# Kernel optimization log

Hardware: AMD Instinct MI355X
Metric: run time of the kernel (lower is better)

Reference implementation:

```python
import math
import jax, jax.numpy as jnp
import numpy as np

B, NW, WH, WW, C, NH = 1024, 64, 8, 8, 512, 8
N = WH * WW
HD = C // NH


def _rel_tables():
    # log-spaced continuous relative coords, shape [(2wh-1)*(2ww-1), 2]
    rh = np.arange(-(WH - 1), WH, dtype=np.float32)
    rw = np.arange(-(WW - 1), WW, dtype=np.float32)
    g = np.stack(np.meshgrid(rh, rw, indexing='ij'), axis=-1)
    norm = np.array([max(WH - 1, 1), max(WW - 1, 1)], dtype=np.float32)
    g = g / norm * 8.0
    g = np.sign(g) * np.log2(np.abs(g) + 1.0) / math.log2(9.0)
    rel_coords = g.reshape(-1, 2).astype(np.float32)
    # relative position index table, shape [N, N]
    ch = np.arange(WH)
    cw = np.arange(WW)
    coords = np.stack(np.meshgrid(ch, cw, indexing='ij')).reshape(2, -1)  # [2, N]
    idx = coords[:, :, None] - coords[:, None, :]  # [2, N, N]
    idx = idx.transpose(1, 2, 0).copy()
    idx[:, :, 0] += WH - 1
    idx[:, :, 1] += WW - 1
    idx[:, :, 0] *= 2 * WW - 1
    rel_idx = idx.sum(-1).astype(np.int32)  # [N, N]
    return jnp.asarray(rel_coords), jnp.asarray(rel_idx)

_REL_COORDS, _REL_IDX = _rel_tables()


def setup_inputs() -> dict:
    key = jax.random.key(0)
    ks = jax.random.split(key, 8)
    x = jax.random.normal(ks[0], (B, N, C), dtype=jnp.float32)
    mask = jnp.zeros((NW, N, N), dtype=jnp.float32)
    qkv_w = jax.random.normal(ks[1], (3 * C, C), dtype=jnp.float32) * 0.02
    q_bias = jnp.zeros((C,), dtype=jnp.float32)
    v_bias = jnp.zeros((C,), dtype=jnp.float32)
    logit_scale = jnp.full((NH, 1, 1), math.log(10.0), dtype=jnp.float32)
    cpb_w1 = jax.random.normal(ks[2], (512, 2), dtype=jnp.float32) * 0.02
    cpb_b1 = jnp.zeros((512,), dtype=jnp.float32)
    cpb_w2 = jax.random.normal(ks[3], (NH, 512), dtype=jnp.float32) * 0.02
    proj_w = jax.random.normal(ks[4], (C, C), dtype=jnp.float32) * 0.02
    proj_b = jnp.zeros((C,), dtype=jnp.float32)
    return {"x": x, "mask": mask, "qkv_w": qkv_w, "q_bias": q_bias,
            "v_bias": v_bias, "logit_scale": logit_scale, "cpb_w1": cpb_w1,
            "cpb_b1": cpb_b1, "cpb_w2": cpb_w2, "proj_w": proj_w,
            "proj_b": proj_b}


def reference(x, mask, qkv_w, q_bias, v_bias, logit_scale,
              cpb_w1, cpb_b1, cpb_w2, proj_w, proj_b):
    # qkv with q/v bias only (k bias is zero)
    bias = jnp.concatenate([q_bias, jnp.zeros_like(v_bias), v_bias])
    qkv = x @ qkv_w.T + bias  # [B, N, 3C]
    qkv = qkv.reshape(B, N, 3, NH, HD).transpose(2, 0, 3, 1, 4)  # [3, B, NH, N, HD]
    q, k, v = qkv[0], qkv[1], qkv[2]
    # cosine-similarity attention with clamped per-head log scale
    q = q / jnp.maximum(jnp.linalg.norm(q, axis=-1, keepdims=True), 1e-12)
    k = k / jnp.maximum(jnp.linalg.norm(k, axis=-1, keepdims=True), 1e-12)
    scale = jnp.exp(jnp.minimum(logit_scale, math.log(100.0)))  # [NH,1,1]
    attn = jnp.einsum('bhnd,bhmd->bhnm', q, k) * scale  # [B, NH, N, N]
    # continuous relative position bias via 2-layer MLP
    cpb = jax.nn.relu(_REL_COORDS @ cpb_w1.T + cpb_b1) @ cpb_w2.T  # [(2wh-1)(2ww-1), NH]
    cpb = 16.0 * jax.nn.sigmoid(cpb)
    bias_mat = cpb[_REL_IDX.reshape(-1)].reshape(N, N, NH).transpose(2, 0, 1)  # [NH, N, N]
    attn = attn + bias_mat[None]
    # window mask add: group windows per image
    attn = attn.reshape(B // NW, NW, NH, N, N) + mask[None, :, None]
    attn = attn.reshape(B, NH, N, N)
    attn = jax.nn.softmax(attn, axis=-1)
    out = jnp.einsum('bhnm,bhmd->bnhd', attn, v).reshape(B, N, C)
    return out @ proj_w.T + proj_b
```

## Files before the change

### kernel.cpp

```cpp
#include <hip/hip_runtime.h>


typedef __bf16 bf16;
typedef bf16  bf16x8 __attribute__((ext_vector_type(8)));
typedef float f32x4  __attribute__((ext_vector_type(4)));

#define MFMA16(a, b, c) __builtin_amdgcn_mfma_f32_16x16x32_bf16((a), (b), (c), 0, 0, 0)

__device__ __forceinline__ unsigned short f2bf_bits(float f) {
  return __builtin_bit_cast(unsigned short, (bf16)f);
}

__device__ __forceinline__ void gload_lds16(const void* g, void* l) {
  __builtin_amdgcn_global_load_lds(
      (const __attribute__((address_space(1))) void*)g,
      (__attribute__((address_space(3))) void*)l, 16, 0, 0);
}

#define OFF_CPB     0u
#define OFF_QKVWT   8192u
#define OFF_PROJWT  1581056u
#define OFF_QHAT    2105344u
#define OFF_KHAT    69214208u
#define OFF_VT      136323072u
#define OFF_ATTN    203431936u
#define OFF_XT      OFF_ATTN

__global__ void wconv_kernel(const float* __restrict__ qkvw,
                             const float* __restrict__ projw,
                             char* __restrict__ ws) {
  int i = blockIdx.x * 256 + threadIdx.x;
#pragma unroll
  for (int it = 0; it < 4; ++it) {
    int idx = i + it * 65536;
    const float* src;
    unsigned base;
    int row, c4;
    if (idx < 196608) {
      row = idx >> 7; c4 = idx & 127;
      src = qkvw + row * 512 + c4 * 4;
      base = OFF_QKVWT + (unsigned)(((row >> 7) * 8 + (c4 >> 4)) << 14);
    } else {
      int j = idx - 196608;
      row = j >> 7; c4 = j & 127;
      src = projw + row * 512 + c4 * 4;
      base = OFF_PROJWT + (unsigned)(((row >> 7) * 8 + (c4 >> 4)) << 14);
    }
    int n = row & 127;
    int kb = (c4 & 15) * 8;
    float4 v = *(const float4*)src;
    ushort4 o;
    o.x = f2bf_bits(v.x); o.y = f2bf_bits(v.y);
    o.z = f2bf_bits(v.z); o.w = f2bf_bits(v.w);
    *(ushort4*)(ws + base + n * 128 + (kb ^ ((n & 7) << 4))) = o;
  }
}

__global__ void xconv_kernel(const float* __restrict__ x, char* __restrict__ ws) {
  int i = blockIdx.x * 1024 + threadIdx.x;
#pragma unroll
  for (int it = 0; it < 4; ++it) {
    int idx = i + it * 256;
    int row = idx >> 7, c4 = idx & 127;
    float4 v = *((const float4*)x + idx);
    ushort4 o;
    o.x = f2bf_bits(v.x); o.y = f2bf_bits(v.y);
    o.z = f2bf_bits(v.z); o.w = f2bf_bits(v.w);
    int n = row & 127;
    int kb = (c4 & 15) * 8;
    size_t base = OFF_XT + ((size_t)((row >> 7) * 8 + (c4 >> 4)) << 14);
    *(ushort4*)(ws + base + n * 128 + (kb ^ ((n & 7) << 4))) = o;
  }
}

__global__ void cpb_kernel(const float* __restrict__ w1, const float* __restrict__ b1,
                           const float* __restrict__ w2, float* __restrict__ cpb_small) {
  const int t = blockIdx.x;
  const int tid = threadIdx.x;
  const int a = t / 15, bb = t % 15;
  const float rh = (float)(a - 7) * (8.0f / 7.0f);
  const float rw = (float)(bb - 7) * (8.0f / 7.0f);
  const float inv_log2_9 = 0.3154648767971186f;
  float sh = (rh > 0.f) ? 1.f : ((rh < 0.f) ? -1.f : 0.f);
  float sw = (rw > 0.f) ? 1.f : ((rw < 0.f) ? -1.f : 0.f);
  float c0 = sh * log2f(fabsf(rh) + 1.0f) * inv_log2_9;
  float c1 = sw * log2f(fabsf(rw) + 1.0f) * inv_log2_9;
  float acc[8] = {0, 0, 0, 0, 0, 0, 0, 0};
  for (int j = tid; j < 512; j += 256) {
    float hv = fmaf(c0, w1[2 * j], fmaf(c1, w1[2 * j + 1], b1[j]));
    hv = fmaxf(hv, 0.0f);
#pragma unroll
    for (int hh = 0; hh < 8; ++hh) acc[hh] = fmaf(hv, w2[hh * 512 + j], acc[hh]);
  }
#pragma unroll
  for (int hh = 0; hh < 8; ++hh)
#pragma unroll
    for (int s = 1; s < 64; s <<= 1) acc[hh] += __shfl_xor(acc[hh], s, 64);
  __shared__ float wsum[4][8];
  if ((tid & 63) == 0) {
#pragma unroll
    for (int hh = 0; hh < 8; ++hh) wsum[tid >> 6][hh] = acc[hh];
  }
  __syncthreads();
  if (tid < 8) {
    float s = wsum[0][tid] + wsum[1][tid] + wsum[2][tid] + wsum[3][tid];
    cpb_small[t * 8 + tid] = 16.0f / (1.0f + expf(-s));
  }
}

__launch_bounds__(256)
__global__ void qkv_gemm(const float* __restrict__ q_bias,
                         const float* __restrict__ v_bias,
                         char* __restrict__ ws) {
  __shared__ __align__(16) char As[16384];
  __shared__ __align__(16) char Bs[16384];
  const int tid = threadIdx.x;
  const int w = tid >> 6, l = tid & 63, lg = l >> 4, lo = l & 15;
  const int wm = w >> 1, wn = w & 1;
  const int bid = blockIdx.x;
  const int wg = (bid & 7) * 768 + (bid >> 3);
  const int mb = wg / 12, nb = wg % 12;

  const char* at_base = ws + OFF_XT + ((size_t)mb * 8 << 14);
  const char* bt_base = ws + OFF_QKVWT + (unsigned)(nb * 8 << 14);

  f32x4 acc[4][4];
#pragma unroll
  for (int mt = 0; mt < 4; ++mt)
#pragma unroll
    for (int nt = 0; nt < 4; ++nt) { f32x4 z = {0.f, 0.f, 0.f, 0.f}; acc[mt][nt] = z; }

#pragma unroll 1
  for (int kc = 0; kc < 8; ++kc) {
    __syncthreads();
    const char* at = at_base + (kc << 14);
    const char* bt = bt_base + (kc << 14);
#pragma unroll
    for (int i = 0; i < 4; ++i) {
      int chunk = i * 4 + w;
      gload_lds16(at + chunk * 1024 + l * 16, As + chunk * 1024);
      gload_lds16(bt + chunk * 1024 + l * 16, Bs + chunk * 1024);
    }
    __syncthreads();
#pragma unroll
    for (int ks = 0; ks < 2; ++ks) {
      bf16x8 af[4], bf[4];
#pragma unroll
      for (int mt = 0; mt < 4; ++mt) {
        int m = wm * 64 + mt * 16 + lo;
        af[mt] = *(const bf16x8*)(As + m * 128 + ((ks * 64 + lg * 16) ^ ((m & 7) << 4)));
      }
#pragma unroll
      for (int nt = 0; nt < 4; ++nt) {
        int n = wn * 64 + nt * 16 + lo;
        bf[nt] = *(const bf16x8*)(Bs + n * 128 + ((ks * 64 + lg * 16) ^ ((n & 7) << 4)));
      }
#pragma unroll
      for (int mt = 0; mt < 4; ++mt)
#pragma unroll
        for (int nt = 0; nt < 4; ++nt)
          acc[mt][nt] = MFMA16(af[mt], bf[nt], acc[mt][nt]);
    }
  }

  const int mat = nb >> 2;
  const int h = ((nb & 3) << 1) + wn;
  const int win = mb * 2 + wm;
  const size_t hb = ((size_t)win * 8 + h) * 4096;

  if (mat != 1) {
    const float* bsrc = (mat == 0) ? q_bias : v_bias;
    float bias[4];
#pragma unroll
    for (int nt = 0; nt < 4; ++nt) bias[nt] = bsrc[h * 64 + nt * 16 + lo];
#pragma unroll
    for (int mt = 0; mt < 4; ++mt)
#pragma unroll
      for (int nt = 0; nt < 4; ++nt)
#pragma unroll
        for (int r = 0; r < 4; ++r) acc[mt][nt][r] += bias[nt];
  }

  if (mat < 2) {
    bf16* dst = (bf16*)(ws + (mat == 0 ? OFF_QHAT : OFF_KHAT)) + hb;
#pragma unroll
    for (int mt = 0; mt < 4; ++mt) {
#pragma unroll
      for (int r = 0; r < 4; ++r) {
        float ss = acc[mt][0][r] * acc[mt][0][r] + acc[mt][1][r] * acc[mt][1][r] +
                   acc[mt][2][r] * acc[mt][2][r] + acc[mt][3][r] * acc[mt][3][r];
#pragma unroll
        for (int s = 1; s < 16; s <<= 1) ss += __shfl_xor(ss, s, 64);
        float rinv = 1.0f / fmaxf(sqrtf(ss), 1e-12f);
        int tok = mt * 16 + lg * 4 + r;
#pragma unroll
        for (int nt = 0; nt < 4; ++nt)
          dst[tok * 64 + nt * 16 + lo] = (bf16)(acc[mt][nt][r] * rinv);
      }
    }
  } else {
    bf16* dst = (bf16*)(ws + OFF_VT) + hb;
#pragma unroll
    for (int mt = 0; mt < 4; ++mt) {
#pragma unroll
      for (int nt = 0; nt < 4; ++nt) {
        ushort4 o;
        o.x = f2bf_bits(acc[mt][nt][0]); o.y = f2bf_bits(acc[mt][nt][1]);
        o.z = f2bf_bits(acc[mt][nt][2]); o.w = f2bf_bits(acc[mt][nt][3]);
        int d = nt * 16 + lo, tok0 = mt * 16 + lg * 4;
        *(ushort4*)(dst + d * 64 + tok0) = o;
      }
    }
  }
}

__launch_bounds__(256)
__global__ void attn_kernel(const float* __restrict__ mask,
                            const float* __restrict__ logit_scale,
                            char* __restrict__ ws) {
  __shared__ float cpbs[1800];
  __shared__ __align__(16) char psb[4][8192];
  const int tid = threadIdx.x;
  const int w = tid >> 6, l = tid & 63, lg = l >> 4, lo = l & 15;
  const int b = blockIdx.x;
  const int widx = b & 63;

  const float* cpb_small = (const float*)(ws + OFF_CPB);
  for (int i = tid; i < 1800; i += 256) cpbs[i] = cpb_small[i];
  __syncthreads();

  const float* mrow = mask + widx * 4096;
  char* pw = psb[w];

#pragma unroll
  for (int hh = 0; hh < 2; ++hh) {
    const int h = w * 2 + hh;
    const size_t hb = ((size_t)b * 8 + h) * 4096;
    const bf16* qh = (const bf16*)(ws + OFF_QHAT) + hb;
    const bf16* kh = (const bf16*)(ws + OFF_KHAT) + hb;
    const bf16* vh = (const bf16*)(ws + OFF_VT) + hb;
    const float scale = __expf(fminf(logit_scale[h], 4.605170185988091f));

    f32x4 sacc[4][4];
#pragma unroll
    for (int mt = 0; mt < 4; ++mt)
#pragma unroll
      for (int nt = 0; nt < 4; ++nt) { f32x4 z = {0.f, 0.f, 0.f, 0.f}; sacc[mt][nt] = z; }
#pragma unroll
    for (int ks = 0; ks < 2; ++ks) {
      bf16x8 a4[4], b4[4];
#pragma unroll
      for (int mt = 0; mt < 4; ++mt)
        a4[mt] = *(const bf16x8*)(qh + (mt * 16 + lo) * 64 + ks * 32 + lg * 8);
#pragma unroll
      for (int nt = 0; nt < 4; ++nt)
        b4[nt] = *(const bf16x8*)(kh + (nt * 16 + lo) * 64 + ks * 32 + lg * 8);
#pragma unroll
      for (int mt = 0; mt < 4; ++mt)
#pragma unroll
        for (int nt = 0; nt < 4; ++nt)
          sacc[mt][nt] = MFMA16(a4[mt], b4[nt], sacc[mt][nt]);
    }

    float invl[4][4];
#pragma unroll
    for (int mt = 0; mt < 4; ++mt) {
#pragma unroll
      for (int r = 0; r < 4; ++r) {
        int row = mt * 16 + lg * 4 + r;
        float sv[4];
#pragma unroll
        for (int nt = 0; nt < 4; ++nt) {
          int col = nt * 16 + lo;
          int idx = ((row >> 3) - (col >> 3) + 7) * 15 + (row & 7) - (col & 7) + 7;
          sv[nt] = fmaf(sacc[mt][nt][r], scale, cpbs[idx * 8 + h] + mrow[row * 64 + col]);
        }
        float mr = fmaxf(fmaxf(sv[0], sv[1]), fmaxf(sv[2], sv[3]));
#pragma unroll
        for (int s = 1; s < 16; s <<= 1) mr = fmaxf(mr, __shfl_xor(mr, s, 64));
        float ls = 0.f;
#pragma unroll
        for (int nt = 0; nt < 4; ++nt) { sv[nt] = __expf(sv[nt] - mr); ls += sv[nt]; }
#pragma unroll
        for (int s = 1; s < 16; s <<= 1) ls += __shfl_xor(ls, s, 64);
        invl[mt][r] = 1.0f / ls;
#pragma unroll
        for (int nt = 0; nt < 4; ++nt)
          *(bf16*)(pw + row * 128 + (((nt * 16 + lo) * 2) ^ ((row & 7) << 4))) = (bf16)sv[nt];
      }
    }
    asm volatile("" ::: "memory");

    f32x4 oacc[4][4];
#pragma unroll
    for (int mt = 0; mt < 4; ++mt)
#pragma unroll
      for (int nt = 0; nt < 4; ++nt) { f32x4 z = {0.f, 0.f, 0.f, 0.f}; oacc[mt][nt] = z; }
#pragma unroll
    for (int ks = 0; ks < 2; ++ks) {
      bf16x8 pa[4], b4[4];
#pragma unroll
      for (int mt = 0; mt < 4; ++mt) {
        int m = mt * 16 + lo;
        pa[mt] = *(const bf16x8*)(pw + m * 128 + ((ks * 64 + lg * 16) ^ ((m & 7) << 4)));
      }
#pragma unroll
      for (int nt = 0; nt < 4; ++nt)
        b4[nt] = *(const bf16x8*)(vh + (nt * 16 + lo) * 64 + ks * 32 + lg * 8);
#pragma unroll
      for (int mt = 0; mt < 4; ++mt)
#pragma unroll
        for (int nt = 0; nt < 4; ++nt)
          oacc[mt][nt] = MFMA16(pa[mt], b4[nt], oacc[mt][nt]);
    }

    char* at = ws + OFF_ATTN + ((size_t)((b >> 1) * 8 + h) << 14);
#pragma unroll
    for (int mt = 0; mt < 4; ++mt) {
#pragma unroll
      for (int r = 0; r < 4; ++r) {
        int rt = (b & 1) * 64 + mt * 16 + lg * 4 + r;
#pragma unroll
        for (int nt = 0; nt < 4; ++nt) {
          int d = nt * 16 + lo;
          *(bf16*)(at + rt * 128 + ((d * 2) ^ ((rt & 7) << 4))) =
              (bf16)(oacc[mt][nt][r] * invl[mt][r]);
        }
      }
    }
    asm volatile("" ::: "memory");
  }
}

__launch_bounds__(256)
__global__ void proj_kernel(const float* __restrict__ proj_b,
                            float* __restrict__ out,
                            const char* __restrict__ ws) {
  __shared__ __align__(16) char As[16384];
  __shared__ __align__(16) char Bs[16384];
  const int tid = threadIdx.x;
  const int w = tid >> 6, l = tid & 63, lg = l >> 4, lo = l & 15;
  const int wm = w >> 1, wn = w & 1;
  const int bid = blockIdx.x;
  const int wg = (bid & 7) * 256 + (bid >> 3);
  const int mb = wg >> 2, nbp = wg & 3;

  const char* at_base = ws + OFF_ATTN + ((size_t)mb * 8 << 14);
  const char* bt_base = ws + OFF_PROJWT + (unsigned)(nbp * 8 << 14);

  f32x4 acc[4][4];
#pragma unroll
  for (int mt = 0; mt < 4; ++mt)
#pragma unroll
    for (int nt = 0; nt < 4; ++nt) { f32x4 z = {0.f, 0.f, 0.f, 0.f}; acc[mt][nt] = z; }

#pragma unroll 1
  for (int kc = 0; kc < 8; ++kc) {
    __syncthreads();
    const char* at = at_base + (kc << 14);
    const char* bt = bt_base + (kc << 14);
#pragma unroll
    for (int i = 0; i < 4; ++i) {
      int chunk = i * 4 + w;
      gload_lds16(at + chunk * 1024 + l * 16, As + chunk * 1024);
      gload_lds16(bt + chunk * 1024 + l * 16, Bs + chunk * 1024);
    }
    __syncthreads();
#pragma unroll
    for (int ks = 0; ks < 2; ++ks) {
      bf16x8 af[4], bf[4];
#pragma unroll
      for (int mt = 0; mt < 4; ++mt) {
        int m = wm * 64 + mt * 16 + lo;
        af[mt] = *(const bf16x8*)(As + m * 128 + ((ks * 64 + lg * 16) ^ ((m & 7) << 4)));
      }
#pragma unroll
      for (int nt = 0; nt < 4; ++nt) {
        int n = wn * 64 + nt * 16 + lo;
        bf[nt] = *(const bf16x8*)(Bs + n * 128 + ((ks * 64 + lg * 16) ^ ((n & 7) << 4)));
      }
#pragma unroll
      for (int mt = 0; mt < 4; ++mt)
#pragma unroll
        for (int nt = 0; nt < 4; ++nt)
          acc[mt][nt] = MFMA16(af[mt], bf[nt], acc[mt][nt]);
    }
  }
#pragma unroll
  for (int nt = 0; nt < 4; ++nt) {
    int col = nbp * 128 + wn * 64 + nt * 16 + lo;
    float pb = proj_b[col];
#pragma unroll
    for (int mt = 0; mt < 4; ++mt) {
#pragma unroll
      for (int r = 0; r < 4; ++r) {
        int row = mb * 128 + wm * 64 + mt * 16 + lg * 4 + r;
        out[(size_t)row * 512 + col] = acc[mt][nt][r] + pb;
      }
    }
  }
}

extern "C" void kernel_launch(void* const* d_in, const int* in_sizes, int n_in,
                              void* d_out, int out_size, void* d_ws, size_t ws_size,
                              hipStream_t stream) {
  const float* x      = (const float*)d_in[0];
  const float* mask   = (const float*)d_in[1];
  const float* qkvw   = (const float*)d_in[2];
  const float* q_bias = (const float*)d_in[3];
  const float* v_bias = (const float*)d_in[4];
  const float* ls     = (const float*)d_in[5];
  const float* cpb_w1 = (const float*)d_in[6];
  const float* cpb_b1 = (const float*)d_in[7];
  const float* cpb_w2 = (const float*)d_in[8];
  const float* proj_w = (const float*)d_in[9];
  const float* proj_b = (const float*)d_in[10];
  float* out = (float*)d_out;
  char* ws = (char*)d_ws;

  hipLaunchKernelGGL(wconv_kernel, dim3(256), dim3(256), 0, stream, qkvw, proj_w, ws);
  hipLaunchKernelGGL(xconv_kernel, dim3(8192), dim3(256), 0, stream, x, ws);
  hipLaunchKernelGGL(cpb_kernel, dim3(225), dim3(256), 0, stream,
                     cpb_w1, cpb_b1, cpb_w2, (float*)(ws + OFF_CPB));
  hipLaunchKernelGGL(qkv_gemm, dim3(6144), dim3(256), 0, stream, q_bias, v_bias, ws);
  hipLaunchKernelGGL(attn_kernel, dim3(1024), dim3(256), 0, stream, mask, ls, ws);
  hipLaunchKernelGGL(proj_kernel, dim3(2048), dim3(256), 0, stream, proj_b, out, ws);
}
```

Measured before the change: 574.5 us.

## Precompute combined bias+mask table and stage attention output through LDS

```diff
diff --git a/kernel.cpp b/kernel.cpp
--- a/kernel.cpp
+++ b/kernel.cpp
@@ -25,6 +25,7 @@
 #define OFF_VT      136323072u
 #define OFF_ATTN    203431936u
 #define OFF_XT      OFF_ATTN
+#define OFF_BM      270540800u
 
 __global__ void wconv_kernel(const float* __restrict__ qkvw,
                              const float* __restrict__ projw,
@@ -108,6 +109,22 @@
   }
 }
 
+__global__ void bmask_kernel(const float* __restrict__ mask,
+                             const float* __restrict__ cpb_small,
+                             float* __restrict__ bm) {
+  const int blk = blockIdx.x;
+  const int widx = blk >> 3, h = blk & 7;
+  const float* mrow = mask + widx * 4096;
+  float* dst = bm + (size_t)blk * 4096;
+#pragma unroll
+  for (int it = 0; it < 16; ++it) {
+    int e = it * 256 + threadIdx.x;
+    int row = e >> 6, col = e & 63;
+    int idx = ((row >> 3) - (col >> 3) + 7) * 15 + ((row & 7) - (col & 7) + 7);
+    dst[e] = cpb_small[idx * 8 + h] + mrow[e];
+  }
+}
+
 __launch_bounds__(256)
 __global__ void qkv_gemm(const float* __restrict__ q_bias,
                          const float* __restrict__ v_bias,
@@ -215,22 +232,15 @@
 }
 
 __launch_bounds__(256)
-__global__ void attn_kernel(const float* __restrict__ mask,
-                            const float* __restrict__ logit_scale,
+__global__ void attn_kernel(const float* __restrict__ logit_scale,
                             char* __restrict__ ws) {
-  __shared__ float cpbs[1800];
   __shared__ __align__(16) char psb[4][8192];
   const int tid = threadIdx.x;
   const int w = tid >> 6, l = tid & 63, lg = l >> 4, lo = l & 15;
   const int b = blockIdx.x;
   const int widx = b & 63;
-
-  const float* cpb_small = (const float*)(ws + OFF_CPB);
-  for (int i = tid; i < 1800; i += 256) cpbs[i] = cpb_small[i];
-  __syncthreads();
-
-  const float* mrow = mask + widx * 4096;
   char* pw = psb[w];
+  const float* bmbase = (const float*)(ws + OFF_BM) + (size_t)widx * 8 * 4096;
 
 #pragma unroll
   for (int hh = 0; hh < 2; ++hh) {
@@ -239,6 +249,7 @@
     const bf16* qh = (const bf16*)(ws + OFF_QHAT) + hb;
     const bf16* kh = (const bf16*)(ws + OFF_KHAT) + hb;
     const bf16* vh = (const bf16*)(ws + OFF_VT) + hb;
+    const float* bmp = bmbase + h * 4096;
     const float scale = __expf(fminf(logit_scale[h], 4.605170185988091f));
 
     f32x4 sacc[4][4];
@@ -270,11 +281,8 @@
         int row = mt * 16 + lg * 4 + r;
         float sv[4];
 #pragma unroll
-        for (int nt = 0; nt < 4; ++nt) {
-          int col = nt * 16 + lo;
-          int idx = ((row >> 3) - (col >> 3) + 7) * 15 + (row & 7) - (col & 7) + 7;
-          sv[nt] = fmaf(sacc[mt][nt][r], scale, cpbs[idx * 8 + h] + mrow[row * 64 + col]);
-        }
+        for (int nt = 0; nt < 4; ++nt)
+          sv[nt] = fmaf(sacc[mt][nt][r], scale, bmp[row * 64 + nt * 16 + lo]);
         float mr = fmaxf(fmaxf(sv[0], sv[1]), fmaxf(sv[2], sv[3]));
 #pragma unroll
         for (int s = 1; s < 16; s <<= 1) mr = fmaxf(mr, __shfl_xor(mr, s, 64));
@@ -313,20 +321,27 @@
         for (int nt = 0; nt < 4; ++nt)
           oacc[mt][nt] = MFMA16(pa[mt], b4[nt], oacc[mt][nt]);
     }
-
-    char* at = ws + OFF_ATTN + ((size_t)((b >> 1) * 8 + h) << 14);
+    asm volatile("" ::: "memory");
+
 #pragma unroll
     for (int mt = 0; mt < 4; ++mt) {
 #pragma unroll
       for (int r = 0; r < 4; ++r) {
-        int rt = (b & 1) * 64 + mt * 16 + lg * 4 + r;
+        int trow = mt * 16 + lg * 4 + r;
 #pragma unroll
         for (int nt = 0; nt < 4; ++nt) {
           int d = nt * 16 + lo;
-          *(bf16*)(at + rt * 128 + ((d * 2) ^ ((rt & 7) << 4))) =
+          *(bf16*)(pw + trow * 128 + ((d * 2) ^ ((trow & 7) << 4))) =
               (bf16)(oacc[mt][nt][r] * invl[mt][r]);
         }
       }
+    }
+    asm volatile("" ::: "memory");
+    char* at2 = ws + OFF_ATTN + ((size_t)((b >> 1) * 8 + h) << 14) + (size_t)(b & 1) * 8192;
+#pragma unroll
+    for (int i = 0; i < 8; ++i) {
+      int off = i * 1024 + l * 16;
+      *(uint4*)(at2 + off) = *(const uint4*)(pw + off);
     }
     asm volatile("" ::: "memory");
   }
@@ -422,7 +437,9 @@
   hipLaunchKernelGGL(xconv_kernel, dim3(8192), dim3(256), 0, stream, x, ws);
   hipLaunchKernelGGL(cpb_kernel, dim3(225), dim3(256), 0, stream,
                      cpb_w1, cpb_b1, cpb_w2, (float*)(ws + OFF_CPB));
+  hipLaunchKernelGGL(bmask_kernel, dim3(512), dim3(256), 0, stream,
+                     mask, (const float*)(ws + OFF_CPB), (float*)(ws + OFF_BM));
   hipLaunchKernelGGL(qkv_gemm, dim3(6144), dim3(256), 0, stream, q_bias, v_bias, ws);
-  hipLaunchKernelGGL(attn_kernel, dim3(1024), dim3(256), 0, stream, mask, ls, ws);
+  hipLaunchKernelGGL(attn_kernel, dim3(1024), dim3(256), 0, stream, ls, ws);
   hipLaunchKernelGGL(proj_kernel, dim3(2048), dim3(256), 0, stream, proj_b, out, ws);
 }
```

Measured after the change: 554.6 us. -3.5%, faster.
